# Kernel optimization log

Measured on AMD Instinct MI355X. Metric: run time of the kernel, lower is better.

Reference implementation:

```python
import jax, jax.numpy as jnp
import numpy as np


def setup_inputs() -> dict:
    key = jax.random.key(0)
    k1, k2 = jax.random.split(key)
    B, Q, P, D = 4, 75, 5, 640  # episodes, queries, prototypes (5-way), feat dim (ResNet-12)
    return {
        "query_feat": jax.random.normal(k1, (B, Q, D), dtype=jnp.float32),
        "proto_feat": jax.random.normal(k2, (B, P, D), dtype=jnp.float32),
    }


def reference(query_feat, proto_feat):
    # Kendall rank correlation (default mode of ProtoLayer).
    # c_pair = combinations(range(D), 2); x[:, c_pair].diff(-1).sign() ==
    # sign(x[..., j] - x[..., i]) for all i < j.
    D = query_feat.shape[-1]
    i_idx, j_idx = np.triu_indices(D, k=1)  # same order as itertools.combinations
    n_pairs = i_idx.shape[0]  # D*(D-1)/2
    q_rank = jnp.sign(query_feat[..., j_idx] - query_feat[..., i_idx])  # (B, Q, n_pairs)
    s_rank = jnp.sign(proto_feat[..., j_idx] - proto_feat[..., i_idx])  # (B, P, n_pairs)
    # per-batch: query_prank @ support_prank.T / n_pairs -> (B, Q, P)
    return jnp.einsum("bqn,bpn->bqp", q_rank, s_rank) / n_pairs
```

## Files before the change

kernel.cpp:

```cpp
#include <hip/hip_runtime.h>
#include <stdint.h>


#define BB 4
#define QQ 75
#define PP 5
#define DD 640
#define NPAIRS 204480
#define NGROUPS 110
#define NROWS_P 20
#define GPW 5
#define NSLOT (NGROUPS / GPW)

__device__ __forceinline__ void pack_bit_v(unsigned& w, float xi_t, float xj) {
    asm("v_cmp_lt_f32 vcc, %1, %2\n\t"
        "v_addc_co_u32 %0, vcc, %0, %0, vcc"
        : "+v"(w)
        : "v"(xi_t), "v"(xj)
        : "vcc");
}

__device__ __forceinline__ unsigned pack_word_lds(const float* __restrict__ sxi,
                                                  float xj, int dlo, int lane) {
    float x[32];
    const float4* __restrict__ v4 = (const float4*)sxi;
#pragma unroll
    for (int u = 0; u < 8; ++u) *(float4*)&x[4 * u] = v4[u];
    unsigned w0 = 0, w1 = 0, w2 = 0, w3 = 0;
#pragma unroll
    for (int t = 0; t < 8; ++t) {
        pack_bit_v(w0, x[t],      xj);
        pack_bit_v(w1, x[t + 8],  xj);
        pack_bit_v(w2, x[t + 16], xj);
        pack_bit_v(w3, x[t + 24], xj);
    }
    unsigned w = (w0 << 24) | (w1 << 16) | (w2 << 8) | w3;
    if (dlo >= 0) {
        const int n = lane - dlo;
        const unsigned msk = (n <= 0) ? 0u
                           : (n >= 32) ? 0xFFFFFFFFu
                                       : (0xFFFFFFFFu << (32 - n));
        w &= msk;
    }
    return w;
}

__device__ __forceinline__ unsigned wave_sum_dpp(unsigned v) {
    v += (unsigned)__builtin_amdgcn_update_dpp(0, (int)v, 0x111, 0xf, 0xf, true);
    v += (unsigned)__builtin_amdgcn_update_dpp(0, (int)v, 0x112, 0xf, 0xf, true);
    v += (unsigned)__builtin_amdgcn_update_dpp(0, (int)v, 0x114, 0xf, 0xf, true);
    v += (unsigned)__builtin_amdgcn_update_dpp(0, (int)v, 0x118, 0xf, 0xf, true);
    v += (unsigned)__builtin_amdgcn_update_dpp(0, (int)v, 0x142, 0xa, 0xf, true);
    v += (unsigned)__builtin_amdgcn_update_dpp(0, (int)v, 0x143, 0xc, 0xf, true);
    return v;
}

__global__ __launch_bounds__(256, 4)
void pack_p(const float* __restrict__ pfeat, unsigned* __restrict__ pm) {
    __shared__ __align__(16) float sp[DD];
    const int tid  = threadIdx.x;
    const int lane = tid & 63;
    const int wave = __builtin_amdgcn_readfirstlane(tid >> 6);
    const int rp   = blockIdx.x;
    const int Gr   = blockIdx.y * 4 + wave;
    const int G    = (Gr < NGROUPS) ? Gr : (NGROUPS - 1);

    if (tid < DD / 4)
        ((float4*)sp)[tid] = ((const float4*)(pfeat + (size_t)rp * DD))[tid];

    int gj = 0;
#pragma unroll 1
    while ((gj + 1) * (gj + 2) <= G) ++gj;
    const int ig = G - gj * (gj + 1);

    __syncthreads();
    if (Gr >= NGROUPS) return;

    const float xj = sp[64 * gj + lane];
    pm[((size_t)G * NROWS_P + rp) * 64 + lane] =
        pack_word_lds(sp + 32 * ig, xj, 32 * ig - 64 * gj, lane);
}

__global__ __launch_bounds__(256, 4)
void kendall(const float* __restrict__ qfeat,
             const unsigned* __restrict__ pm,
             float* __restrict__ out) {
    __shared__ __align__(16) float sx[DD];
    const int tid  = threadIdx.x;
    const int lane = tid & 63;
    const int wave = __builtin_amdgcn_readfirstlane(tid >> 6);
    const int bq   = blockIdx.x;
    const int sl4  = blockIdx.y * 4 + wave;
    const int slot = (sl4 < NSLOT) ? sl4 : (NSLOT - 1);
    const int b    = bq / QQ;

    if (tid < DD / 4)
        ((float4*)sx)[tid] = ((const float4*)(qfeat + (size_t)bq * DD))[tid];

    const int G0 = GPW * slot;
    int gj = 0;
#pragma unroll 1
    while ((gj + 1) * (gj + 2) <= G0) ++gj;
    int ig = G0 - gj * (gj + 1);

    int gjs[GPW], igs[GPW];
#pragma unroll
    for (int k = 0; k < GPW; ++k) {
        gjs[k] = gj; igs[k] = ig;
        if (++ig == 2 * gj + 2) { ++gj; ig = 0; }
    }

    unsigned pr[GPW][PP];
#pragma unroll
    for (int k = 0; k < GPW; ++k) {
        const unsigned* __restrict__ pw =
            pm + ((size_t)(G0 + k) * NROWS_P + b * PP) * 64 + lane;
#pragma unroll
        for (int p = 0; p < PP; ++p) pr[k][p] = pw[p * 64];
    }

    __syncthreads();
    if (sl4 >= NSLOT) return;

    unsigned m0 = 0, m1 = 0, m2 = 0, m3 = 0, m4 = 0;

#pragma unroll
    for (int k = 0; k < GPW; ++k) {
        const float xj = sx[64 * gjs[k] + lane];
        const unsigned qw = pack_word_lds(sx + 32 * igs[k], xj,
                                          32 * igs[k] - 64 * gjs[k], lane);
        m0 += __popc(qw ^ pr[k][0]);
        m1 += __popc(qw ^ pr[k][1]);
        m2 += __popc(qw ^ pr[k][2]);
        m3 += __popc(qw ^ pr[k][3]);
        m4 += __popc(qw ^ pr[k][4]);
    }

    const unsigned s01 = wave_sum_dpp(m0 | (m1 << 16));
    const unsigned s23 = wave_sum_dpp(m2 | (m3 << 16));
    const unsigned s4  = wave_sum_dpp(m4);
    const unsigned c01 = (unsigned)__builtin_amdgcn_readlane((int)s01, 63);
    const unsigned c23 = (unsigned)__builtin_amdgcn_readlane((int)s23, 63);
    const unsigned c4  = (unsigned)__builtin_amdgcn_readlane((int)s4,  63);

    if (lane == 0) {
        const float base = (slot == 0) ? 1.0f : 0.0f;
        const float s = -2.0f / (float)NPAIRS;
        float* o = out + (size_t)bq * PP;
        atomicAdd(o + 0, base + s * (float)(c01 & 0xFFFFu));
        atomicAdd(o + 1, base + s * (float)(c01 >> 16));
        atomicAdd(o + 2, base + s * (float)(c23 & 0xFFFFu));
        atomicAdd(o + 3, base + s * (float)(c23 >> 16));
        atomicAdd(o + 4, base + s * (float)c4);
    }
}

extern "C" void kernel_launch(void* const* d_in, const int* in_sizes, int n_in,
                              void* d_out, int out_size, void* d_ws, size_t ws_size,
                              hipStream_t stream) {
    const float* qfeat = (const float*)d_in[0];
    const float* pfeat = (const float*)d_in[1];
    float* out = (float*)d_out;
    unsigned* pm = (unsigned*)d_ws;

    pack_p <<<dim3(NROWS_P, 28), 256, 0, stream>>>(pfeat, pm);
    kendall<<<dim3(BB * QQ, 6),  256, 0, stream>>>(qfeat, pm, out);
}
```

Baseline: 68.48 us.

## Fuse prototype packing into Kendall kernel and share packed prototype words via LDS

Removes the separate pack_p launch and its global workspace round-trip. Each block now loads one episode's prototypes and four query rows into LDS. It packs the prototype sign-bit words for its slot group itself and keeps them in LDS for the popcount loop. Work is regrouped so each wave handles one query row for one slot of five groups. The cost is redundant prototype packing in every block, extra LDS traffic and barriers, and wasted lanes for the padded last quad.

```diff
diff --git a/kernel.cpp b/kernel.cpp
--- a/kernel.cpp
+++ b/kernel.cpp
@@ -8,9 +8,10 @@
 #define DD 640
 #define NPAIRS 204480
 #define NGROUPS 110
-#define NROWS_P 20
 #define GPW 5
 #define NSLOT (NGROUPS / GPW)
+#define QUADS 19
+#define NPW (GPW * PP)
 
 __device__ __forceinline__ void pack_bit_v(unsigned& w, float xi_t, float xj) {
     asm("v_cmp_lt_f32 vcc, %1, %2\n\t"
@@ -55,54 +56,66 @@
     return v;
 }
 
-__global__ __launch_bounds__(256, 4)
-void pack_p(const float* __restrict__ pfeat, unsigned* __restrict__ pm) {
-    __shared__ __align__(16) float sp[DD];
+__global__ __launch_bounds__(256, 7)
+void kendall_fused(const float* __restrict__ qfeat,
+                   const float* __restrict__ pfeat,
+                   float* __restrict__ out) {
+    __shared__ __align__(16) float smem[4 * DD + PP * DD];
+    float*    const sq   = smem;
+    float*    const sp   = smem + 4 * DD;
+    unsigned* const plds = (unsigned*)(smem + 4 * DD);
+
     const int tid  = threadIdx.x;
     const int lane = tid & 63;
     const int wave = __builtin_amdgcn_readfirstlane(tid >> 6);
-    const int rp   = blockIdx.x;
-    const int Gr   = blockIdx.y * 4 + wave;
-    const int G    = (Gr < NGROUPS) ? Gr : (NGROUPS - 1);
+    const int b    = blockIdx.x / QUADS;
+    const int quad = blockIdx.x - b * QUADS;
+    const int slot = blockIdx.y;
+    const int G0   = GPW * slot;
 
-    if (tid < DD / 4)
-        ((float4*)sp)[tid] = ((const float4*)(pfeat + (size_t)rp * DD))[tid];
+    if (tid < DD / 4) {
+#pragma unroll
+        for (int qi = 0; qi < 4; ++qi) {
+            const int lr = 4 * quad + qi;
+            const int rr = (lr < QQ) ? lr : (QQ - 1);
+            ((float4*)(sq + qi * DD))[tid] =
+                ((const float4*)(qfeat + ((size_t)b * QQ + rr) * DD))[tid];
+        }
+    }
+    const float4* __restrict__ p4 = (const float4*)(pfeat + (size_t)b * PP * DD);
+#pragma unroll 1
+    for (int i = tid; i < PP * DD / 4; i += 256)
+        ((float4*)sp)[i] = p4[i];
+    __syncthreads();
+
+    unsigned pw[7];
+#pragma unroll
+    for (int c = 0; c < 7; ++c) {
+        const int widx = wave + 4 * c;
+        const int wc   = (widx < NPW) ? widx : (NPW - 1);
+        const int kk   = wc / 5;
+        const int p    = wc - 5 * kk;
+        const int G    = G0 + kk;
+        int gjw = 0;
+        while ((gjw + 1) * (gjw + 2) <= G) ++gjw;
+        const int igw = G - gjw * (gjw + 1);
+        const float* __restrict__ prow = sp + p * DD;
+        pw[c] = pack_word_lds(prow + 32 * igw, prow[64 * gjw + lane],
+                              32 * igw - 64 * gjw, lane);
+    }
+    __syncthreads();
+
+#pragma unroll
+    for (int c = 0; c < 7; ++c) {
+        const int widx = wave + 4 * c;
+        if (widx < NPW)
+            plds[widx * 64 + lane] = pw[c];
+    }
+    __syncthreads();
 
     int gj = 0;
-#pragma unroll 1
-    while ((gj + 1) * (gj + 2) <= G) ++gj;
-    const int ig = G - gj * (gj + 1);
-
-    __syncthreads();
-    if (Gr >= NGROUPS) return;
-
-    const float xj = sp[64 * gj + lane];
-    pm[((size_t)G * NROWS_P + rp) * 64 + lane] =
-        pack_word_lds(sp + 32 * ig, xj, 32 * ig - 64 * gj, lane);
-}
-
-__global__ __launch_bounds__(256, 4)
-void kendall(const float* __restrict__ qfeat,
-             const unsigned* __restrict__ pm,
-             float* __restrict__ out) {
-    __shared__ __align__(16) float sx[DD];
-    const int tid  = threadIdx.x;
-    const int lane = tid & 63;
-    const int wave = __builtin_amdgcn_readfirstlane(tid >> 6);
-    const int bq   = blockIdx.x;
-    const int sl4  = blockIdx.y * 4 + wave;
-    const int slot = (sl4 < NSLOT) ? sl4 : (NSLOT - 1);
-    const int b    = bq / QQ;
-
-    if (tid < DD / 4)
-        ((float4*)sx)[tid] = ((const float4*)(qfeat + (size_t)bq * DD))[tid];
-
-    const int G0 = GPW * slot;
-    int gj = 0;
-#pragma unroll 1
     while ((gj + 1) * (gj + 2) <= G0) ++gj;
     int ig = G0 - gj * (gj + 1);
-
     int gjs[GPW], igs[GPW];
 #pragma unroll
     for (int k = 0; k < GPW; ++k) {
@@ -110,30 +123,21 @@
         if (++ig == 2 * gj + 2) { ++gj; ig = 0; }
     }
 
-    unsigned pr[GPW][PP];
+    const int  lrow   = 4 * quad + wave;
+    const bool active = (lrow < QQ);
+    const float* __restrict__ srow = sq + wave * DD;
+
+    unsigned m0 = 0, m1 = 0, m2 = 0, m3 = 0, m4 = 0;
 #pragma unroll
     for (int k = 0; k < GPW; ++k) {
-        const unsigned* __restrict__ pw =
-            pm + ((size_t)(G0 + k) * NROWS_P + b * PP) * 64 + lane;
-#pragma unroll
-        for (int p = 0; p < PP; ++p) pr[k][p] = pw[p * 64];
-    }
-
-    __syncthreads();
-    if (sl4 >= NSLOT) return;
-
-    unsigned m0 = 0, m1 = 0, m2 = 0, m3 = 0, m4 = 0;
-
-#pragma unroll
-    for (int k = 0; k < GPW; ++k) {
-        const float xj = sx[64 * gjs[k] + lane];
-        const unsigned qw = pack_word_lds(sx + 32 * igs[k], xj,
+        const float xj = srow[64 * gjs[k] + lane];
+        const unsigned qw = pack_word_lds(srow + 32 * igs[k], xj,
                                           32 * igs[k] - 64 * gjs[k], lane);
-        m0 += __popc(qw ^ pr[k][0]);
-        m1 += __popc(qw ^ pr[k][1]);
-        m2 += __popc(qw ^ pr[k][2]);
-        m3 += __popc(qw ^ pr[k][3]);
-        m4 += __popc(qw ^ pr[k][4]);
+        m0 += __popc(qw ^ plds[(k * 5 + 0) * 64 + lane]);
+        m1 += __popc(qw ^ plds[(k * 5 + 1) * 64 + lane]);
+        m2 += __popc(qw ^ plds[(k * 5 + 2) * 64 + lane]);
+        m3 += __popc(qw ^ plds[(k * 5 + 3) * 64 + lane]);
+        m4 += __popc(qw ^ plds[(k * 5 + 4) * 64 + lane]);
     }
 
     const unsigned s01 = wave_sum_dpp(m0 | (m1 << 16));
@@ -143,7 +147,8 @@
     const unsigned c23 = (unsigned)__builtin_amdgcn_readlane((int)s23, 63);
     const unsigned c4  = (unsigned)__builtin_amdgcn_readlane((int)s4,  63);
 
-    if (lane == 0) {
+    if (lane == 0 && active) {
+        const int bq = b * QQ + lrow;
         const float base = (slot == 0) ? 1.0f : 0.0f;
         const float s = -2.0f / (float)NPAIRS;
         float* o = out + (size_t)bq * PP;
@@ -161,8 +166,7 @@
     const float* qfeat = (const float*)d_in[0];
     const float* pfeat = (const float*)d_in[1];
     float* out = (float*)d_out;
-    unsigned* pm = (unsigned*)d_ws;
+    (void)d_ws; (void)ws_size;
 
-    pack_p <<<dim3(NROWS_P, 28), 256, 0, stream>>>(pfeat, pm);
-    kendall<<<dim3(BB * QQ, 6),  256, 0, stream>>>(qfeat, pm, out);
+    kendall_fused<<<dim3(BB * QUADS, NSLOT), 256, 0, stream>>>(qfeat, pfeat, out);
 }
```

Result: slower. 70.40 us (+2.8%).
